# Optimization experiments

Hardware: AMD Instinct MI355X
Metric: run time of the kernel (lower is better)

Reference implementation:

```python
import jax, jax.numpy as jnp
import numpy as np

K = 10  # num_neighbors in original nn_index call


def setup_inputs() -> dict:
    key = jax.random.key(0)
    k1, k2, k3, k4 = jax.random.split(key, 4)
    B, OBS, ACT, N = 256, 32, 2, 500000
    obs = jax.random.normal(k1, (B, OBS), dtype=jnp.float32)
    action = jax.random.normal(k2, (B, ACT), dtype=jnp.float32)
    mem_sa = jax.random.normal(k3, (N, OBS + ACT), dtype=jnp.float32)
    mem_Q = jax.random.normal(k4, (N, 1), dtype=jnp.float32)
    return {"obs": obs, "action": action, "mem_sa": mem_sa, "mem_Q": mem_Q}


def reference(obs, action, mem_sa, mem_Q):
    # query: [B, D] state-action, brute-force kNN over memory table [N, D]
    q = jnp.concatenate([obs, action], axis=1)
    # squared Euclidean distances (FLANN returns squared L2): [B, N]
    d2 = (jnp.sum(q * q, axis=1, keepdims=True)
          - 2.0 * q @ mem_sa.T
          + jnp.sum(mem_sa * mem_sa, axis=1)[None, :])
    neg_d, idx = jax.lax.top_k(-d2, K)   # nearest K neighbors
    dists = -neg_d                        # [B, K], ascending
    Qs = mem_Q[idx, 0]                    # gather Q values: [B, K]
    # NOTE: original applies softmax to raw distances (not negated)
    weights = jax.nn.softmax(dists, axis=1)
    return jnp.sum(weights * Qs, axis=1)  # [B]
```

## Files before the change

kernel.cpp:

```cpp
#include <hip/hip_runtime.h>
#include <math.h>

#define NPTS   500000
#define NB     256
#define TOPK   10
#define CAP    2048
#define SBLK   1024
#define SPER   16
#define MARGIN 2.0f
#define FBLK   768
#define NCHUNK 3907
#define LCAP   8
#define QSR    40
#define PMAIN  393216
#define OCAP   65536

typedef short v4s  __attribute__((ext_vector_type(4)));
typedef short v8s  __attribute__((ext_vector_type(8)));
typedef float v16f __attribute__((ext_vector_type(16)));

__device__ __forceinline__ unsigned short f2bf(float f) {
    unsigned u = __float_as_uint(f);
    unsigned r = u + 0x7FFFu + ((u >> 16) & 1u);
    return (unsigned short)(r >> 16);
}
__device__ __forceinline__ float bf2f(unsigned short h) {
    return __uint_as_float(((unsigned)h) << 16);
}
__device__ __forceinline__ float bf2fs(short h) {
    return __uint_as_float(((unsigned)(unsigned short)h) << 16);
}

__device__ __forceinline__ float norm34(const float* __restrict__ r) {
    float a0 = 0.f, a1 = 0.f, a2 = 0.f, a3 = 0.f;
#pragma unroll
    for (int d = 0; d < 32; d += 4) {
        a0 = fmaf(r[d + 0], r[d + 0], a0);
        a1 = fmaf(r[d + 1], r[d + 1], a1);
        a2 = fmaf(r[d + 2], r[d + 2], a2);
        a3 = fmaf(r[d + 3], r[d + 3], a3);
    }
    a0 = fmaf(r[32], r[32], a0);
    a1 = fmaf(r[33], r[33], a1);
    return (a0 + a1) + (a2 + a3);
}
__device__ __forceinline__ float dot34(const float* __restrict__ r, const float* q) {
    float a0 = 0.f, a1 = 0.f, a2 = 0.f, a3 = 0.f;
#pragma unroll
    for (int d = 0; d < 32; d += 4) {
        a0 = fmaf(r[d + 0], q[d + 0], a0);
        a1 = fmaf(r[d + 1], q[d + 1], a1);
        a2 = fmaf(r[d + 2], q[d + 2], a2);
        a3 = fmaf(r[d + 3], q[d + 3], a3);
    }
    a0 = fmaf(r[32], q[32], a0);
    a1 = fmaf(r[33], q[33], a1);
    return (a0 + a1) + (a2 + a3);
}
__device__ __forceinline__ float dot34_v4(const float4* __restrict__ r4, const float* q) {
    float a0 = 0.f, a1 = 0.f, a2 = 0.f, a3 = 0.f;
#pragma unroll
    for (int dp = 0; dp < 8; ++dp) {
        float4 v = r4[dp];
        a0 = fmaf(v.x, q[4 * dp + 0], a0);
        a1 = fmaf(v.y, q[4 * dp + 1], a1);
        a2 = fmaf(v.z, q[4 * dp + 2], a2);
        a3 = fmaf(v.w, q[4 * dp + 3], a3);
    }
    float2 t = *(const float2*)(r4 + 8);
    a0 = fmaf(t.x, q[32], a0);
    a1 = fmaf(t.y, q[33], a1);
    return (a0 + a1) + (a2 + a3);
}
__device__ __forceinline__ void load_q(const float* __restrict__ obs,
                                       const float* __restrict__ act, int b, float* q) {
#pragma unroll
    for (int d = 0; d < 32; ++d) q[d] = obs[b * 32 + d];
    q[32] = act[b * 2 + 0];
    q[33] = act[b * 2 + 1];
}

__global__ __launch_bounds__(256, 4) void k_sample(const float* __restrict__ obs,
                                                   const float* __restrict__ act,
                                                   const float* __restrict__ msa,
                                                   float* __restrict__ minima) {
    __shared__ __align__(16) float sm[SPER * 36];
    __shared__ float smn[SPER];
    const int g = blockIdx.x, t = threadIdx.x;
    const int base = g * SPER;
    for (int i = t; i < SPER * 34; i += 256) {
        int row = i / 34, d = i - row * 34;
        sm[row * 36 + d] = msa[(size_t)base * 34 + i];
    }
    __syncthreads();
    if (t < SPER) smn[t] = norm34(&sm[t * 36]);
    __syncthreads();
    float q[34];
    load_q(obs, act, t, q);
    float best = __builtin_inff();
#pragma unroll
    for (int j = 0; j < SPER; ++j) {
        float s = fmaf(-2.f, dot34_v4((const float4*)&sm[j * 36], q), smn[j]);
        best = fminf(best, s);
    }
    minima[(size_t)t * SBLK + g] = best;
}

__global__ __launch_bounds__(64) void k_tau(const float* __restrict__ minima,
                                            const float* __restrict__ obs,
                                            const float* __restrict__ act,
                                            unsigned short* __restrict__ qbf,
                                            int* __restrict__ cursor) {
    const int b = blockIdx.x, lane = threadIdx.x;
    if (b == 0 && lane == 0) { cursor[0] = 0; cursor[1] = 0; }
    float v[16];
#pragma unroll
    for (int k = 0; k < 16; ++k) v[k] = minima[(size_t)b * SBLK + lane + 64 * k];
    float last = 0.f;
    for (int r = 0; r < TOPK; ++r) {
        float lm = v[0]; int la = 0;
#pragma unroll
        for (int k = 1; k < 16; ++k) { if (v[k] < lm) { lm = v[k]; la = k; } }
        float wm = lm;
        for (int off = 32; off; off >>= 1) wm = fminf(wm, __shfl_xor(wm, off));
        unsigned long long msk = __ballot(lm == wm);
        int first = (int)__builtin_ctzll(msk);
        if (lane == first) {
#pragma unroll
            for (int k = 0; k < 16; ++k) { if (k == la) v[k] = __builtin_inff(); }
        }
        last = wm;
    }
    float val = 0.f;
    if (lane < 32)       val = obs[b * 32 + lane];
    else if (lane < 34)  val = act[b * 2 + (lane - 32)];
    else if (lane == 34) val = -0.5f;
    else if (lane == 35) val = 0.5f * (last + MARGIN);
    if (lane < QSR) qbf[b * QSR + lane] = (lane < 36) ? f2bf(val) : (unsigned short)0;
}

__global__ __launch_bounds__(256, 4) void k_filter(const float* __restrict__ msa,
                                                   const unsigned short* __restrict__ qbf,
                                                   int* __restrict__ cursor,
                                                   unsigned* __restrict__ pbuf,
                                                   int* __restrict__ posq) {
    __shared__ __align__(16) unsigned short lq[NB * QSR];
    __shared__ __align__(16) unsigned short lm[128 * QSR];
    __shared__ int lcount[NB];
    __shared__ int lcand[NB * LCAP];
    __shared__ int gbase;
    const int g = blockIdx.x, t = threadIdx.x;
    lcount[t] = 0;
    const float4* qsrc = (const float4*)qbf;
    for (int i = t; i < NB * QSR / 8; i += 256)
        *(float4*)&lq[i * 8] = qsrc[i];
    const int w = t >> 6, lane = t & 63;
    const int mrow = lane & 31, half = lane >> 5;
    const v8s vz8 = (v8s)(short)0;
    for (int c = g; c < NCHUNK; c += FBLK) {
        const int lo = c * 128;
        __syncthreads();
        for (int i = t; i < 128 * 17; i += 256) {
            int row = i / 17, dp = i - row * 17;
            int gp = lo + row;
            float2 v = make_float2(0.f, 0.f);
            if (gp < NPTS) v = *(const float2*)&msa[(size_t)gp * 34 + 2 * dp];
            ushort2 h; h.x = f2bf(v.x); h.y = f2bf(v.y);
            *(ushort2*)&lm[row * QSR + 2 * dp] = h;
        }
        __syncthreads();
        const unsigned short* mr = &lm[(w * 32 + mrow) * QSR];
        const int p = lo + w * 32 + mrow;
        float nrm = 0.f;
#pragma unroll
        for (int dp4 = 0; dp4 < 8; ++dp4) {
            v4s h4 = *(const v4s*)(mr + 4 * dp4);
            nrm = fmaf(bf2fs(h4[0]), bf2fs(h4[0]), nrm);
            nrm = fmaf(bf2fs(h4[1]), bf2fs(h4[1]), nrm);
            nrm = fmaf(bf2fs(h4[2]), bf2fs(h4[2]), nrm);
            nrm = fmaf(bf2fs(h4[3]), bf2fs(h4[3]), nrm);
        }
        ushort2 h33 = *(const ushort2*)(mr + 32);
        nrm = fmaf(bf2f(h33.x), bf2f(h33.x), nrm);
        nrm = fmaf(bf2f(h33.y), bf2f(h33.y), nrm);
        if (p >= NPTS) nrm = 1e30f;
        v8s B0 = *(const v8s*)(mr + half * 8);
        v8s B1 = *(const v8s*)(mr + 16 + half * 8);
        v8s B2 = vz8;
        if (half == 0) {
            B2[0] = (short)h33.x;
            B2[1] = (short)h33.y;
            B2[2] = (short)f2bf(nrm);
            B2[3] = (short)0x3F80;
        }
#pragma unroll
        for (int qt = 0; qt < 8; ++qt) {
            const unsigned short* qr = &lq[(qt * 32 + mrow) * QSR];
            v8s A0 = *(const v8s*)(qr + half * 8);
            v8s A1 = *(const v8s*)(qr + 16 + half * 8);
            v8s A2 = vz8;
            if (half == 0) A2 = *(const v8s*)(qr + 32);
            v16f acc;
#pragma unroll
            for (int i = 0; i < 16; ++i) acc[i] = 0.f;
            acc = __builtin_amdgcn_mfma_f32_32x32x16_bf16(A0, B0, acc, 0, 0, 0);
            acc = __builtin_amdgcn_mfma_f32_32x32x16_bf16(A1, B1, acc, 0, 0, 0);
            acc = __builtin_amdgcn_mfma_f32_32x32x16_bf16(A2, B2, acc, 0, 0, 0);
            unsigned hm = 0;
#pragma unroll
            for (int r = 0; r < 16; ++r) hm |= (acc[r] >= 0.f) ? (1u << r) : 0u;
            while (hm) {
                int r = __builtin_ctz(hm);
                hm &= hm - 1;
                int qq = qt * 32 + (r & 3) + 8 * (r >> 2) + 4 * half;
                int slot = atomicAdd(&lcount[qq], 1);
                if (slot < LCAP) {
                    lcand[qq * LCAP + slot] = p;
                } else {
                    int dg = atomicAdd(cursor + 1, 1);
                    if (dg < OCAP) pbuf[PMAIN + dg] = ((unsigned)qq << 19) | (unsigned)p;
                }
            }
        }
    }
    __syncthreads();
    int n = lcount[t];
    if (n > LCAP) n = LCAP;
    lcount[t] = n;
    __syncthreads();
    for (int off = 1; off < 256; off <<= 1) {
        int v = (t >= off) ? lcount[t - off] : 0;
        __syncthreads();
        lcount[t] += v;
        __syncthreads();
    }
    int base_l = lcount[t] - n;
    if (t == 255) gbase = atomicAdd(cursor, lcount[255]);
    __syncthreads();
    int start = gbase + base_l;
    if (start + n > PMAIN) n = (start < PMAIN) ? (PMAIN - start) : 0;
    posq[g * NB + t] = start | (n << 20);
    for (int i = 0; i < n; ++i)
        pbuf[start + i] = (unsigned)lcand[t * LCAP + i];
}

__global__ __launch_bounds__(256) void k_final(const float* __restrict__ obs,
                                               const float* __restrict__ act,
                                               const float* __restrict__ msa,
                                               const unsigned* __restrict__ pbuf,
                                               const int* __restrict__ posq,
                                               const int* __restrict__ cursor,
                                               const float* __restrict__ memQ,
                                               float* __restrict__ out) {
    __shared__ float ls[CAP];
    __shared__ int   li[CAP];
    __shared__ int   lcnt;
    __shared__ float rs[4];
    __shared__ int   ri[4];
    __shared__ float sel_s[TOPK];
    __shared__ int   sel_i[TOPK];
    const int b = blockIdx.x, t = threadIdx.x;
    const int lane = t & 63, wid = t >> 6;
    if (t == 0) lcnt = 0;
    __syncthreads();
    for (int g = t; g < FBLK; g += 256) {
        int packed = posq[g * NB + b];
        int n = (packed >> 20) & 0xF;
        int pos = packed & 0xFFFFF;
        if (n > 0) {
            int base = atomicAdd(&lcnt, n);
            for (int i = 0; i < n; ++i) {
                int dst = base + i;
                if (dst < CAP) li[dst] = (int)pbuf[pos + i];
            }
        }
    }
    int novf = cursor[1];
    if (novf > OCAP) novf = OCAP;
    for (int j = t; j < novf; j += 256) {
        unsigned pr = pbuf[PMAIN + j];
        if ((int)(pr >> 19) == b) {
            int s = atomicAdd(&lcnt, 1);
            if (s < CAP) li[s] = (int)(pr & 0x7FFFFu);
        }
    }
    __syncthreads();
    int cnt = lcnt;
    if (cnt > CAP) cnt = CAP;
    float q[34];
    load_q(obs, act, b, q);
    for (int j = t; j < cnt; j += 256) {
        const float* row = msa + (size_t)li[j] * 34;
        ls[j] = fmaf(-2.f, dot34(row, q), norm34(row));
    }
    __syncthreads();
    for (int k = 0; k < TOPK; ++k) {
        float bs = __builtin_inff();
        int   bi = 0x7fffffff;
        for (int j = t; j < cnt; j += 256) {
            float s = ls[j]; int i = li[j];
            if (s < bs || (s == bs && i < bi)) { bs = s; bi = i; }
        }
        for (int off = 32; off; off >>= 1) {
            float s2 = __shfl_down(bs, off);
            int   i2 = __shfl_down(bi, off);
            if (s2 < bs || (s2 == bs && i2 < bi)) { bs = s2; bi = i2; }
        }
        if (lane == 0) { rs[wid] = bs; ri[wid] = bi; }
        __syncthreads();
        if (t == 0) {
            float fs = rs[0]; int fi = ri[0];
#pragma unroll
            for (int ww = 1; ww < 4; ++ww) {
                if (rs[ww] < fs || (rs[ww] == fs && ri[ww] < fi)) { fs = rs[ww]; fi = ri[ww]; }
            }
            sel_s[k] = fs; sel_i[k] = fi;
        }
        __syncthreads();
        const int win = sel_i[k];
        for (int j = t; j < cnt; j += 256) {
            if (li[j] == win) ls[j] = __builtin_inff();
        }
        __syncthreads();
    }
    if (t == 0) {
        float m = sel_s[TOPK - 1];
        float wsum = 0.f, acc = 0.f;
#pragma unroll
        for (int k = 0; k < TOPK; ++k) {
            if (sel_i[k] == 0x7fffffff) continue;
            float w2 = expf(sel_s[k] - m);
            wsum += w2;
            acc = fmaf(w2, memQ[sel_i[k]], acc);
        }
        out[b] = acc / wsum;
    }
}

extern "C" void kernel_launch(void* const* d_in, const int* in_sizes, int n_in,
                              void* d_out, int out_size, void* d_ws, size_t ws_size,
                              hipStream_t stream) {
    const float* obs = (const float*)d_in[0];
    const float* act = (const float*)d_in[1];
    const float* msa = (const float*)d_in[2];
    const float* mq  = (const float*)d_in[3];
    float* out = (float*)d_out;

    char* ws = (char*)d_ws;
    unsigned short* qbf = (unsigned short*)ws;
    int*      cursor = (int*)(ws + 20480);
    float*    minima = (float*)(ws + 32768);
    int*      posq   = (int*)(ws + 32768 + 1048576);
    unsigned* pbuf   = (unsigned*)(ws + 32768 + 1048576 + 786432);

    k_sample<<<SBLK, 256, 0, stream>>>(obs, act, msa, minima);
    k_tau   <<<NB, 64, 0, stream>>>(minima, obs, act, qbf, cursor);
    k_filter<<<FBLK, 256, 0, stream>>>(msa, qbf, cursor, pbuf, posq);
    k_final <<<NB, 256, 0, stream>>>(obs, act, msa, pbuf, posq, cursor, mq, out);
}
```

Baseline: 186.5 us.

## Async-copy memory tiles to LDS and prebuild MFMA query fragments globally

The filter kernel now copies fp32 memory rows straight into LDS with global_load_lds and converts them to bf16 in registers. The query tile is no longer staged in LDS: k_tau writes ready-made MFMA A-fragments that each wave loads directly. This lowers LDS use, so occupancy goes to 5 blocks and the grid grows to 1280. k_final replaces its atomic gather of candidates with a prefix-sum over 5 posq entries per thread. It also adds per-iteration global fragment loads and a larger posq buffer.

```diff
diff --git a/kernel.cpp b/kernel.cpp
--- a/kernel.cpp
+++ b/kernel.cpp
@@ -1,4 +1,5 @@
 #include <hip/hip_runtime.h>
+#include <hip/hip_bf16.h>
 #include <math.h>
 
 #define NPTS   500000
@@ -8,12 +9,11 @@
 #define SBLK   1024
 #define SPER   16
 #define MARGIN 2.0f
-#define FBLK   768
+#define FBLK   1280
 #define NCHUNK 3907
 #define LCAP   8
-#define QSR    40
 #define PMAIN  393216
-#define OCAP   65536
+#define OCAP   32768
 
 typedef short v4s  __attribute__((ext_vector_type(4)));
 typedef short v8s  __attribute__((ext_vector_type(8)));
@@ -27,8 +27,11 @@
 __device__ __forceinline__ float bf2f(unsigned short h) {
     return __uint_as_float(((unsigned)h) << 16);
 }
-__device__ __forceinline__ float bf2fs(short h) {
-    return __uint_as_float(((unsigned)(unsigned short)h) << 16);
+
+__device__ __forceinline__ void async_copy16(void* lds, const void* g) {
+    __builtin_amdgcn_global_load_lds(
+        (const __attribute__((address_space(1))) unsigned*)g,
+        (__attribute__((address_space(3))) unsigned*)lds, 16, 0, 0);
 }
 
 __device__ __forceinline__ float norm34(const float* __restrict__ r) {
@@ -109,8 +112,9 @@
 __global__ __launch_bounds__(64) void k_tau(const float* __restrict__ minima,
                                             const float* __restrict__ obs,
                                             const float* __restrict__ act,
-                                            unsigned short* __restrict__ qbf,
+                                            v8s* __restrict__ afrag,
                                             int* __restrict__ cursor) {
+    __shared__ __align__(16) unsigned short qs[48];
     const int b = blockIdx.x, lane = threadIdx.x;
     if (b == 0 && lane == 0) { cursor[0] = 0; cursor[1] = 0; }
     float v[16];
@@ -136,70 +140,76 @@
     else if (lane < 34)  val = act[b * 2 + (lane - 32)];
     else if (lane == 34) val = -0.5f;
     else if (lane == 35) val = 0.5f * (last + MARGIN);
-    if (lane < QSR) qbf[b * QSR + lane] = (lane < 36) ? f2bf(val) : (unsigned short)0;
-}
-
-__global__ __launch_bounds__(256, 4) void k_filter(const float* __restrict__ msa,
-                                                   const unsigned short* __restrict__ qbf,
+    if (lane < 48) qs[lane] = (lane < 36) ? f2bf(val) : (unsigned short)0;
+    __syncthreads();
+    if (lane < 6) {
+        int s = lane >> 1, half = lane & 1;
+        int qt = b >> 5, mrow = b & 31;
+        v8s frag = *(const v8s*)&qs[s * 16 + half * 8];
+        afrag[(qt * 3 + s) * 64 + half * 32 + mrow] = frag;
+    }
+}
+
+__global__ __launch_bounds__(256, 5) void k_filter(const float* __restrict__ msa,
+                                                   const v8s* __restrict__ afrag,
                                                    int* __restrict__ cursor,
                                                    unsigned* __restrict__ pbuf,
                                                    int* __restrict__ posq) {
-    __shared__ __align__(16) unsigned short lq[NB * QSR];
-    __shared__ __align__(16) unsigned short lm[128 * QSR];
+    __shared__ __align__(16) float lmf[128 * 34];
     __shared__ int lcount[NB];
     __shared__ int lcand[NB * LCAP];
     __shared__ int gbase;
     const int g = blockIdx.x, t = threadIdx.x;
-    lcount[t] = 0;
-    const float4* qsrc = (const float4*)qbf;
-    for (int i = t; i < NB * QSR / 8; i += 256)
-        *(float4*)&lq[i * 8] = qsrc[i];
     const int w = t >> 6, lane = t & 63;
     const int mrow = lane & 31, half = lane >> 5;
-    const v8s vz8 = (v8s)(short)0;
+    lcount[t] = 0;
     for (int c = g; c < NCHUNK; c += FBLK) {
         const int lo = c * 128;
         __syncthreads();
-        for (int i = t; i < 128 * 17; i += 256) {
-            int row = i / 17, dp = i - row * 17;
-            int gp = lo + row;
-            float2 v = make_float2(0.f, 0.f);
-            if (gp < NPTS) v = *(const float2*)&msa[(size_t)gp * 34 + 2 * dp];
-            ushort2 h; h.x = f2bf(v.x); h.y = f2bf(v.y);
-            *(ushort2*)&lm[row * QSR + 2 * dp] = h;
-        }
-        __syncthreads();
-        const unsigned short* mr = &lm[(w * 32 + mrow) * QSR];
+        if (lo + 128 <= NPTS) {
+            const char* src = (const char*)(msa + (size_t)lo * 34);
+            char* dst = (char*)lmf;
+            for (int seg = w; seg < 17; seg += 4)
+                async_copy16(dst + seg * 1024 + lane * 16, src + seg * 1024 + lane * 16);
+        } else {
+            const int valid = NPTS - lo;
+            for (int i = t; i < 128 * 34; i += 256) lmf[i] = 0.f;
+            __syncthreads();
+            for (int i = t; i < valid * 34; i += 256) lmf[i] = msa[(size_t)lo * 34 + i];
+        }
+        __syncthreads();
+        const float* myrow = &lmf[(w * 32 + mrow) * 34];
         const int p = lo + w * 32 + mrow;
-        float nrm = 0.f;
-#pragma unroll
-        for (int dp4 = 0; dp4 < 8; ++dp4) {
-            v4s h4 = *(const v4s*)(mr + 4 * dp4);
-            nrm = fmaf(bf2fs(h4[0]), bf2fs(h4[0]), nrm);
-            nrm = fmaf(bf2fs(h4[1]), bf2fs(h4[1]), nrm);
-            nrm = fmaf(bf2fs(h4[2]), bf2fs(h4[2]), nrm);
-            nrm = fmaf(bf2fs(h4[3]), bf2fs(h4[3]), nrm);
-        }
-        ushort2 h33 = *(const ushort2*)(mr + 32);
-        nrm = fmaf(bf2f(h33.x), bf2f(h33.x), nrm);
-        nrm = fmaf(bf2f(h33.y), bf2f(h33.y), nrm);
+        unsigned pk[17];
+        float n0 = 0.f, n1 = 0.f;
+#pragma unroll
+        for (int i = 0; i < 17; ++i) {
+            float2 f2 = *(const float2*)(myrow + 2 * i);
+            __hip_bfloat162 b2 = __float22bfloat162_rn(f2);
+            unsigned u = *(unsigned*)&b2;
+            pk[i] = u;
+            float r0 = bf2f((unsigned short)(u & 0xFFFFu));
+            float r1 = bf2f((unsigned short)(u >> 16));
+            n0 = fmaf(r0, r0, n0);
+            n1 = fmaf(r1, r1, n1);
+        }
+        float nrm = n0 + n1;
         if (p >= NPTS) nrm = 1e30f;
-        v8s B0 = *(const v8s*)(mr + half * 8);
-        v8s B1 = *(const v8s*)(mr + 16 + half * 8);
-        v8s B2 = vz8;
+        union U { unsigned u[4]; v8s v; };
+        U b0, b1, b2u;
+#pragma unroll
+        for (int i = 0; i < 4; ++i) { b0.u[i] = pk[half * 4 + i]; b1.u[i] = pk[8 + half * 4 + i]; }
+        b2u.u[0] = 0; b2u.u[1] = 0; b2u.u[2] = 0; b2u.u[3] = 0;
         if (half == 0) {
-            B2[0] = (short)h33.x;
-            B2[1] = (short)h33.y;
-            B2[2] = (short)f2bf(nrm);
-            B2[3] = (short)0x3F80;
-        }
+            b2u.u[0] = pk[16];
+            b2u.u[1] = (unsigned)f2bf(nrm) | (0x3F80u << 16);
+        }
+        const v8s B0 = b0.v, B1 = b1.v, B2 = b2u.v;
 #pragma unroll
         for (int qt = 0; qt < 8; ++qt) {
-            const unsigned short* qr = &lq[(qt * 32 + mrow) * QSR];
-            v8s A0 = *(const v8s*)(qr + half * 8);
-            v8s A1 = *(const v8s*)(qr + 16 + half * 8);
-            v8s A2 = vz8;
-            if (half == 0) A2 = *(const v8s*)(qr + 32);
+            v8s A0 = afrag[(qt * 3 + 0) * 64 + lane];
+            v8s A1 = afrag[(qt * 3 + 1) * 64 + lane];
+            v8s A2 = afrag[(qt * 3 + 2) * 64 + lane];
             v16f acc;
 #pragma unroll
             for (int i = 0; i < 16; ++i) acc[i] = 0.f;
@@ -238,7 +248,8 @@
     if (t == 255) gbase = atomicAdd(cursor, lcount[255]);
     __syncthreads();
     int start = gbase + base_l;
-    if (start + n > PMAIN) n = (start < PMAIN) ? (PMAIN - start) : 0;
+    if (start >= PMAIN) { start = 0; n = 0; }
+    else if (start + n > PMAIN) n = PMAIN - start;
     posq[g * NB + t] = start | (n << 20);
     for (int i = 0; i < n; ++i)
         pbuf[start + i] = (unsigned)lcand[t * LCAP + i];
@@ -254,6 +265,7 @@
                                                float* __restrict__ out) {
     __shared__ float ls[CAP];
     __shared__ int   li[CAP];
+    __shared__ int   sc[NB];
     __shared__ int   lcnt;
     __shared__ float rs[4];
     __shared__ int   ri[4];
@@ -261,20 +273,31 @@
     __shared__ int   sel_i[TOPK];
     const int b = blockIdx.x, t = threadIdx.x;
     const int lane = t & 63, wid = t >> 6;
-    if (t == 0) lcnt = 0;
-    __syncthreads();
-    for (int g = t; g < FBLK; g += 256) {
-        int packed = posq[g * NB + b];
-        int n = (packed >> 20) & 0xF;
-        int pos = packed & 0xFFFFF;
-        if (n > 0) {
-            int base = atomicAdd(&lcnt, n);
-            for (int i = 0; i < n; ++i) {
-                int dst = base + i;
-                if (dst < CAP) li[dst] = (int)pbuf[pos + i];
-            }
-        }
-    }
+    int nk[5], pk5[5], tot = 0;
+#pragma unroll
+    for (int k = 0; k < 5; ++k) {
+        int packed = posq[(size_t)(t + 256 * k) * NB + b];
+        nk[k] = (packed >> 20) & 0xF;
+        pk5[k] = packed & 0xFFFFF;
+        tot += nk[k];
+    }
+    sc[t] = tot;
+    __syncthreads();
+    for (int off = 1; off < 256; off <<= 1) {
+        int v = (t >= off) ? sc[t - off] : 0;
+        __syncthreads();
+        sc[t] += v;
+        __syncthreads();
+    }
+    int myoff = sc[t] - tot;
+    if (t == 0) lcnt = (sc[255] > CAP) ? CAP : sc[255];
+    __syncthreads();
+#pragma unroll
+    for (int k = 0; k < 5; ++k)
+        for (int i = 0; i < nk[k]; ++i) {
+            if (myoff < CAP) li[myoff] = (int)pbuf[pk5[k] + i];
+            ++myoff;
+        }
     int novf = cursor[1];
     if (novf > OCAP) novf = OCAP;
     for (int j = t; j < novf; j += 256) {
@@ -347,14 +370,14 @@
     float* out = (float*)d_out;
 
     char* ws = (char*)d_ws;
-    unsigned short* qbf = (unsigned short*)ws;
-    int*      cursor = (int*)(ws + 20480);
+    int*      cursor = (int*)ws;
+    v8s*      afrag  = (v8s*)(ws + 256);
     float*    minima = (float*)(ws + 32768);
     int*      posq   = (int*)(ws + 32768 + 1048576);
-    unsigned* pbuf   = (unsigned*)(ws + 32768 + 1048576 + 786432);
+    unsigned* pbuf   = (unsigned*)(ws + 32768 + 1048576 + 1310720);
 
     k_sample<<<SBLK, 256, 0, stream>>>(obs, act, msa, minima);
-    k_tau   <<<NB, 64, 0, stream>>>(minima, obs, act, qbf, cursor);
-    k_filter<<<FBLK, 256, 0, stream>>>(msa, qbf, cursor, pbuf, posq);
+    k_tau   <<<NB, 64, 0, stream>>>(minima, obs, act, afrag, cursor);
+    k_filter<<<FBLK, 256, 0, stream>>>(msa, afrag, cursor, pbuf, posq);
     k_final <<<NB, 256, 0, stream>>>(obs, act, msa, pbuf, posq, cursor, mq, out);
 }
```

Result: slower. 232.7 us (+24.8%).
